# Optimization experiments

Hardware: AMD Instinct MI355X
Metric: run time of the kernel (lower is better)

## Reference

```python
import jax, jax.numpy as jnp
import numpy as np

N, E, F_IN, H, C = 169343, 1166243, 128, 128, 40
BN_EPS = 1e-5


def setup_inputs() -> dict:
    key = jax.random.key(0)
    ks = jax.random.split(key, 16)
    inp = {
        "x": jax.random.normal(ks[0], (N, F_IN), jnp.float32),
        "edge_index": jax.random.randint(ks[1], (2, E), 0, N, dtype=jnp.int64),
        "W1": jax.random.normal(ks[2], (F_IN, H), jnp.float32) * (1.0 / np.sqrt(F_IN)),
        "b1": jnp.zeros((H,), jnp.float32),
        "g1": jnp.ones((H,), jnp.float32),
        "be1": jnp.zeros((H,), jnp.float32),
        "m1": jax.random.normal(ks[3], (H,), jnp.float32) * 0.1,
        "v1": jax.random.uniform(ks[4], (H,), jnp.float32, 0.5, 1.5),
        "W2": jax.random.normal(ks[5], (H, H), jnp.float32) * (1.0 / np.sqrt(H)),
        "b2": jnp.zeros((H,), jnp.float32),
        "g2": jnp.ones((H,), jnp.float32),
        "be2": jnp.zeros((H,), jnp.float32),
        "m2": jax.random.normal(ks[6], (H,), jnp.float32) * 0.1,
        "v2": jax.random.uniform(ks[7], (H,), jnp.float32, 0.5, 1.5),
        "W3": jax.random.normal(ks[8], (H, C), jnp.float32) * (1.0 / np.sqrt(H)),
        "b3": jnp.zeros((C,), jnp.float32),
    }
    return inp


def _gcn_conv(h, W, b, src, dst, norm, n_nodes):
    # GCNConv: out = D^-1/2 (A+I) D^-1/2 (h W) + b
    hw = h @ W                                   # [N, H] dense GEMM
    msgs = hw[src] * norm[:, None]               # [E', H] gather (irregular)
    agg = jax.ops.segment_sum(msgs, dst, num_segments=n_nodes)  # scatter-add
    return agg + b


def _bn_eval(h, gamma, beta, mean, var):
    return (h - mean) * jax.lax.rsqrt(var + BN_EPS) * gamma + beta


def reference(x, edge_index, W1, b1, g1, be1, m1, v1,
              W2, b2, g2, be2, m2, v2, W3, b3):
    n = x.shape[0]
    loops = jnp.arange(n, dtype=edge_index.dtype)
    src = jnp.concatenate([edge_index[0], loops])  # add self-loops
    dst = jnp.concatenate([edge_index[1], loops])
    deg = jax.ops.segment_sum(jnp.ones_like(dst, dtype=x.dtype), dst, num_segments=n)
    dinv = jax.lax.rsqrt(jnp.maximum(deg, 1.0))
    norm = dinv[src] * dinv[dst]                  # [E+N]

    # layer stack (eval mode: dropout is identity, repeated ReLU idempotent)
    h = jax.nn.relu(_gcn_conv(x, W1, b1, src, dst, norm, n))
    h = jax.nn.relu(_bn_eval(h, g1, be1, m1, v1))
    h = jax.nn.relu(_gcn_conv(h, W2, b2, src, dst, norm, n))
    h = jax.nn.relu(_bn_eval(h, g2, be2, m2, v2))
    out = h @ W3 + b3                              # final Linear [N, C]
    return jax.nn.log_softmax(out, axis=-1), jnp.var(out, ddof=1)
```

## Files before the change

kernel.cpp:

```cpp
#include <hip/hip_runtime.h>
#include <math.h>

#define BN_EPS 1e-5f

typedef _Float16 f16;
typedef __attribute__((ext_vector_type(4))) _Float16 f16x4;
typedef __attribute__((ext_vector_type(8))) _Float16 f16x8;
typedef __attribute__((ext_vector_type(4))) float f32x4;

__device__ __forceinline__ int edge_at(const void* ei, long long idx, int is64) {
    if (is64) return (int)((const long long*)ei)[idx];
    return ((const int*)ei)[idx];
}

__global__ void init_kernel(const void* ei, int* flag, int* deg_i,
                            double* scal, int* done, int n) {
    int i = blockIdx.x * 256 + threadIdx.x;
    if (i < n) deg_i[i] = 0;
    if (blockIdx.x == 0 && threadIdx.x == 0) {
        scal[0] = 0.0; scal[1] = 0.0;
        *done = 0;
        const int* p = (const int*)ei;
        int f = 1;
        for (int k = 0; k < 64; k++)
            if (p[2 * k + 1] != 0) { f = 0; break; }
        *flag = f;
    }
}

__global__ void degi_kernel(const void* ei, const int* flag, int* deg_i,
                            int* __restrict__ rank, int E) {
    const int base = blockIdx.x * 1024 + threadIdx.x;
    const int is64 = *flag;
    #pragma unroll
    for (int k = 0; k < 4; k++) {
        int e = base + k * 256;
        if (e < E) {
            int d = edge_at(ei, (long long)E + e, is64);
            rank[e] = atomicAdd(&deg_i[d], 1);
        }
    }
}

__global__ __launch_bounds__(256) void scan1_kernel(
    const int* __restrict__ in, int* __restrict__ excl, int* bsum, int n) {
    __shared__ int sh[256];
    const int tid = threadIdx.x;
    const int base = blockIdx.x * 2048 + tid * 8;
    int v[8];
    #pragma unroll
    for (int i = 0; i < 8; i++) v[i] = (base + i < n) ? in[base + i] : 0;
    int tsum = 0;
    #pragma unroll
    for (int i = 0; i < 8; i++) { int t = v[i]; v[i] = tsum; tsum += t; }
    sh[tid] = tsum;
    __syncthreads();
    for (int off = 1; off < 256; off <<= 1) {
        int t = 0;
        if (tid >= off) t = sh[tid - off];
        __syncthreads();
        if (tid >= off) sh[tid] += t;
        __syncthreads();
    }
    int texcl = sh[tid] - tsum;
    #pragma unroll
    for (int i = 0; i < 8; i++)
        if (base + i < n) excl[base + i] = texcl + v[i];
    if (tid == 255 && bsum) bsum[blockIdx.x] = sh[255];
}

__global__ void scan3_kernel(int* rowptr, const int* __restrict__ boff,
                             const int* __restrict__ deg_i,
                             float* __restrict__ dinv, int n, int E) {
    int i = blockIdx.x * 256 + threadIdx.x;
    if (i < n) {
        rowptr[i] = rowptr[i] + boff[i >> 11];
        dinv[i] = rsqrtf((float)(deg_i[i] + 1));
    }
    if (i == 0) rowptr[n] = E;
}

__global__ void fill_kernel(const void* ei, const int* flag,
                            const int* __restrict__ rowptr,
                            const int* __restrict__ rank,
                            int* __restrict__ col, int E) {
    const int base = blockIdx.x * 1024 + threadIdx.x;
    const int is64 = *flag;
    #pragma unroll
    for (int k = 0; k < 4; k++) {
        int e = base + k * 256;
        if (e < E) {
            int s = edge_at(ei, e, is64);
            int d = edge_at(ei, (long long)E + e, is64);
            __builtin_nontemporal_store(s, &col[rowptr[d] + rank[e]]);
        }
    }
}

__global__ __launch_bounds__(256) void prep_w_kernel(
    const float* __restrict__ W1, f16* __restrict__ Wt1h, f16* __restrict__ Wt1l,
    const float* __restrict__ W2, f16* __restrict__ Wt2h, f16* __restrict__ Wt2l) {
    for (int f = blockIdx.x * 256 + threadIdx.x; f < 2 * 128 * 128;
         f += gridDim.x * 256) {
        int which = f >> 14, g = f & 16383;
        int k = g >> 7, nn = g & 127;
        const float* W = which ? W2 : W1;
        f16* Wh = which ? Wt2h : Wt1h;
        f16* Wl = which ? Wt2l : Wt1l;
        float wv = W[g];
        f16 h = (f16)wv;
        Wh[nn * 128 + k] = h;
        Wl[nn * 128 + k] = (f16)(wv - (float)h);
    }
}

#define APAD 40
__global__ __launch_bounds__(256) void gemm_l1_kernel(
    const float* __restrict__ X, const f16* __restrict__ Wth,
    const f16* __restrict__ Wtl, const float* __restrict__ dinv,
    f16* __restrict__ out, int M) {
    __shared__ f16 Ah[128 * APAD];
    __shared__ f16 Bh[128 * APAD];
    __shared__ f16 Bl[128 * APAD];
    const int t = threadIdx.x;
    const int r0 = blockIdx.x * 128;
    const int w = t >> 6, lane = t & 63;
    const int m0 = (w >> 1) * 64, n0 = (w & 1) * 64;
    const int fr = lane & 15;
    const int kb = (lane >> 4) * 8;

    f32x4 acc[4][4];
    #pragma unroll
    for (int i = 0; i < 4; i++)
        #pragma unroll
        for (int j = 0; j < 4; j++) acc[i][j] = (f32x4)0.f;

    for (int k0 = 0; k0 < 128; k0 += 32) {
        #pragma unroll
        for (int i = 0; i < 4; i++) {
            int f = t + i * 256;
            int row = f >> 3, kq = (f & 7) * 4;
            float4 v = make_float4(0.f, 0.f, 0.f, 0.f);
            if (r0 + row < M)
                v = *(const float4*)&X[(size_t)(r0 + row) * 128 + k0 + kq];
            *(f16x4*)&Ah[row * APAD + kq] =
                (f16x4){(f16)v.x, (f16)v.y, (f16)v.z, (f16)v.w};
        }
        #pragma unroll
        for (int i = 0; i < 2; i++) {
            int f = t + i * 256;
            int nrow = f >> 2, kq = (f & 3) * 8;
            int gb = nrow * 128 + k0 + kq;
            int lb = nrow * APAD + kq;
            *(uint4*)&Bh[lb] = *(const uint4*)&Wth[gb];
            *(uint4*)&Bl[lb] = *(const uint4*)&Wtl[gb];
        }
        __syncthreads();

        f16x8 a0[4], b0[4], xx[4];
        #pragma unroll
        for (int i = 0; i < 4; i++) {
            a0[i] = *(const f16x8*)&Ah[(m0 + i * 16 + fr) * APAD + kb];
            b0[i] = *(const f16x8*)&Bh[(n0 + i * 16 + fr) * APAD + kb];
        }
        #pragma unroll
        for (int i = 0; i < 4; i++)
            #pragma unroll
            for (int j = 0; j < 4; j++)
                acc[i][j] = __builtin_amdgcn_mfma_f32_16x16x32_f16(
                    a0[i], b0[j], acc[i][j], 0, 0, 0);
        #pragma unroll
        for (int i = 0; i < 4; i++)
            xx[i] = *(const f16x8*)&Bl[(n0 + i * 16 + fr) * APAD + kb];
        #pragma unroll
        for (int i = 0; i < 4; i++)
            #pragma unroll
            for (int j = 0; j < 4; j++)
                acc[i][j] = __builtin_amdgcn_mfma_f32_16x16x32_f16(
                    a0[i], xx[j], acc[i][j], 0, 0, 0);
        __syncthreads();
    }

    #pragma unroll
    for (int i = 0; i < 4; i++) {
        #pragma unroll
        for (int r = 0; r < 4; r++) {
            int row = r0 + m0 + i * 16 + (lane >> 4) * 4 + r;
            if (row < M) {
                float di = dinv[row];
                #pragma unroll
                for (int j = 0; j < 4; j++)
                    out[(size_t)row * 128 + n0 + j * 16 + fr] =
                        (f16)(acc[i][j][r] * di);
            }
        }
    }
}

__global__ __launch_bounds__(256) void gemm_l2_kernel(
    const f16* __restrict__ X, const f16* __restrict__ Wth,
    const f16* __restrict__ Wtl, const float* __restrict__ dinv,
    f16* __restrict__ out, int M) {
    __shared__ f16 Ax[128 * APAD];
    __shared__ f16 Bh[128 * APAD];
    __shared__ f16 Bl[128 * APAD];
    const int t = threadIdx.x;
    const int r0 = blockIdx.x * 128;
    const int w = t >> 6, lane = t & 63;
    const int m0 = (w >> 1) * 64, n0 = (w & 1) * 64;
    const int fr = lane & 15;
    const int kb = (lane >> 4) * 8;

    f32x4 acc[4][4];
    #pragma unroll
    for (int i = 0; i < 4; i++)
        #pragma unroll
        for (int j = 0; j < 4; j++) acc[i][j] = (f32x4)0.f;

    for (int k0 = 0; k0 < 128; k0 += 32) {
        #pragma unroll
        for (int i = 0; i < 2; i++) {
            int f = t + i * 256;
            int row = f >> 2, kq = (f & 3) * 8;
            uint4 v = make_uint4(0u, 0u, 0u, 0u);
            if (r0 + row < M)
                v = *(const uint4*)&X[(size_t)(r0 + row) * 128 + k0 + kq];
            *(uint4*)&Ax[row * APAD + kq] = v;
        }
        #pragma unroll
        for (int i = 0; i < 2; i++) {
            int f = t + i * 256;
            int nrow = f >> 2, kq = (f & 3) * 8;
            int gb = nrow * 128 + k0 + kq;
            int lb = nrow * APAD + kq;
            *(uint4*)&Bh[lb] = *(const uint4*)&Wth[gb];
            *(uint4*)&Bl[lb] = *(const uint4*)&Wtl[gb];
        }
        __syncthreads();

        f16x8 a0[4], b0[4], xx[4];
        #pragma unroll
        for (int i = 0; i < 4; i++) {
            a0[i] = *(const f16x8*)&Ax[(m0 + i * 16 + fr) * APAD + kb];
            b0[i] = *(const f16x8*)&Bh[(n0 + i * 16 + fr) * APAD + kb];
        }
        #pragma unroll
        for (int i = 0; i < 4; i++)
            #pragma unroll
            for (int j = 0; j < 4; j++)
                acc[i][j] = __builtin_amdgcn_mfma_f32_16x16x32_f16(
                    a0[i], b0[j], acc[i][j], 0, 0, 0);
        #pragma unroll
        for (int i = 0; i < 4; i++)
            xx[i] = *(const f16x8*)&Bl[(n0 + i * 16 + fr) * APAD + kb];
        #pragma unroll
        for (int i = 0; i < 4; i++)
            #pragma unroll
            for (int j = 0; j < 4; j++)
                acc[i][j] = __builtin_amdgcn_mfma_f32_16x16x32_f16(
                    a0[i], xx[j], acc[i][j], 0, 0, 0);
        __syncthreads();
    }

    #pragma unroll
    for (int i = 0; i < 4; i++) {
        #pragma unroll
        for (int r = 0; r < 4; r++) {
            int row = r0 + m0 + i * 16 + (lane >> 4) * 4 + r;
            if (row < M) {
                float di = dinv[row];
                #pragma unroll
                for (int j = 0; j < 4; j++)
                    out[(size_t)row * 128 + n0 + j * 16 + fr] =
                        (f16)(acc[i][j][r] * di);
            }
        }
    }
}

__global__ __launch_bounds__(256) void agg_kernel(
    const f16* __restrict__ hs, const int* __restrict__ rowptr,
    const int* __restrict__ col, const float* __restrict__ dinv,
    const float* __restrict__ b, const float* __restrict__ g,
    const float* __restrict__ be, const float* __restrict__ m,
    const float* __restrict__ v, f16* __restrict__ h, int M) {
    const int node = blockIdx.x * 8 + (threadIdx.x >> 5);
    if (node >= M) return;
    const int lane = threadIdx.x & 31;
    const int c = lane * 4;
    const f16* __restrict__ base = hs + c;

    f16x4 sv = *(const f16x4*)&base[(size_t)node * 128];
    float a0[4] = {(float)sv[0], (float)sv[1], (float)sv[2], (float)sv[3]};
    float a1[4] = {0.f, 0.f, 0.f, 0.f};
    float a2[4] = {0.f, 0.f, 0.f, 0.f};
    float a3[4] = {0.f, 0.f, 0.f, 0.f};
    const int beg = rowptr[node], end = rowptr[node + 1];
    int j = beg;
    for (; j + 3 < end; j += 4) {
        int s0 = col[j], s1 = col[j + 1], s2 = col[j + 2], s3 = col[j + 3];
        f16x4 v0 = *(const f16x4*)&base[(size_t)s0 * 128];
        f16x4 v1 = *(const f16x4*)&base[(size_t)s1 * 128];
        f16x4 v2 = *(const f16x4*)&base[(size_t)s2 * 128];
        f16x4 v3 = *(const f16x4*)&base[(size_t)s3 * 128];
        #pragma unroll
        for (int q = 0; q < 4; q++) {
            a0[q] += (float)v0[q]; a1[q] += (float)v1[q];
            a2[q] += (float)v2[q]; a3[q] += (float)v3[q];
        }
    }
    if (j + 1 < end) {
        int s0 = col[j], s1 = col[j + 1];
        f16x4 v0 = *(const f16x4*)&base[(size_t)s0 * 128];
        f16x4 v1 = *(const f16x4*)&base[(size_t)s1 * 128];
        #pragma unroll
        for (int q = 0; q < 4; q++) { a0[q] += (float)v0[q]; a1[q] += (float)v1[q]; }
        j += 2;
    }
    if (j < end) {
        int s0 = col[j];
        f16x4 v0 = *(const f16x4*)&base[(size_t)s0 * 128];
        #pragma unroll
        for (int q = 0; q < 4; q++) a0[q] += (float)v0[q];
    }
    const float di = dinv[node];
    f16x4 r;
    #pragma unroll
    for (int q = 0; q < 4; q++) {
        int cc = c + q;
        float s = (a0[q] + a1[q]) + (a2[q] + a3[q]);
        float tt = fmaxf(di * s + b[cc], 0.f);
        tt = (tt - m[cc]) * (g[cc] * rsqrtf(v[cc] + BN_EPS)) + be[cc];
        r[q] = (f16)fmaxf(tt, 0.f);
    }
    *(f16x4*)&h[(size_t)node * 128 + c] = r;
}

__global__ __launch_bounds__(256) void gemm_out_kernel(
    const f16* __restrict__ H, const float* __restrict__ W3,
    const float* __restrict__ b3, float* __restrict__ out,
    double* __restrict__ scal, int* __restrict__ done, int M) {
    __shared__ float Hs[256][20];
    __shared__ float Ws[128][40];
    const int t  = threadIdx.x;
    const int r0 = blockIdx.x * 256;
    #pragma unroll
    for (int i = 0; i < 5; i++) {
        int f = t + i * 256;
        ((float4*)Ws)[f] = ((const float4*)W3)[f];
    }
    const int rg = t >> 2;
    const int cb = (t & 3) * 10;
    float acc[4][10];
    #pragma unroll
    for (int i = 0; i < 4; i++)
        #pragma unroll
        for (int j = 0; j < 10; j++) acc[i][j] = 0.f;

    for (int k0 = 0; k0 < 128; k0 += 16) {
        __syncthreads();
        #pragma unroll
        for (int i = 0; i < 4; i++) {
            int f = t + i * 256;
            int r = f >> 2, c4 = (f & 3) * 4;
            float4 hv = make_float4(0.f, 0.f, 0.f, 0.f);
            if (r0 + r < M) {
                f16x4 hx = *(const f16x4*)&H[(size_t)(r0 + r) * 128 + k0 + c4];
                hv = make_float4((float)hx[0], (float)hx[1],
                                 (float)hx[2], (float)hx[3]);
            }
            *(float4*)&Hs[r][c4] = hv;
        }
        __syncthreads();
        #pragma unroll
        for (int k4 = 0; k4 < 4; k4++) {
            float hv[4][4];
            #pragma unroll
            for (int i = 0; i < 4; i++) {
                float4 h4 = *(const float4*)&Hs[rg + 64 * i][k4 * 4];
                hv[i][0] = h4.x; hv[i][1] = h4.y; hv[i][2] = h4.z; hv[i][3] = h4.w;
            }
            #pragma unroll
            for (int q = 0; q < 4; q++) {
                int k = k0 + k4 * 4 + q;
                float wv[10];
                #pragma unroll
                for (int j = 0; j < 5; j++) {
                    float2 w2 = *(const float2*)&Ws[k][cb + 2 * j];
                    wv[2 * j] = w2.x; wv[2 * j + 1] = w2.y;
                }
                #pragma unroll
                for (int i = 0; i < 4; i++)
                    #pragma unroll
                    for (int j = 0; j < 10; j++)
                        acc[i][j] = fmaf(hv[i][q], wv[j], acc[i][j]);
            }
        }
    }

    float s1 = 0.f, s2 = 0.f;
    #pragma unroll
    for (int i = 0; i < 4; i++) {
        int row = r0 + rg + 64 * i;
        float vb[10];
        #pragma unroll
        for (int j = 0; j < 10; j++) vb[j] = acc[i][j] + b3[cb + j];
        float mx = vb[0];
        #pragma unroll
        for (int j = 1; j < 10; j++) mx = fmaxf(mx, vb[j]);
        mx = fmaxf(mx, __shfl_xor(mx, 1));
        mx = fmaxf(mx, __shfl_xor(mx, 2));
        float se = 0.f;
        #pragma unroll
        for (int j = 0; j < 10; j++) se += expf(vb[j] - mx);
        se += __shfl_xor(se, 1);
        se += __shfl_xor(se, 2);
        float ls = mx + logf(se);
        if (row < M) {
            #pragma unroll
            for (int j = 0; j < 10; j++) {
                out[(size_t)row * 40 + cb + j] = vb[j] - ls;
                s1 += vb[j];
                s2 += vb[j] * vb[j];
            }
        }
    }
    #pragma unroll
    for (int o = 32; o; o >>= 1) { s1 += __shfl_xor(s1, o); s2 += __shfl_xor(s2, o); }
    __shared__ double sh1[4], sh2[4];
    if ((t & 63) == 0) { sh1[t >> 6] = (double)s1; sh2[t >> 6] = (double)s2; }
    __syncthreads();
    if (t == 0) {
        atomicAdd(&scal[0], sh1[0] + sh1[1] + sh1[2] + sh1[3]);
        atomicAdd(&scal[1], sh2[0] + sh2[1] + sh2[2] + sh2[3]);
        __threadfence();
        int prev = atomicAdd(done, 1);
        if (prev == (int)gridDim.x - 1) {
            __threadfence();
            double t1 = atomicAdd(&scal[0], 0.0);
            double t2 = atomicAdd(&scal[1], 0.0);
            long long nn = (long long)M * 40;
            out[nn] = (float)((t2 - t1 * t1 / (double)nn) / (double)(nn - 1));
        }
    }
}

extern "C" void kernel_launch(void* const* d_in, const int* in_sizes, int n_in,
                              void* d_out, int out_size, void* d_ws, size_t ws_size,
                              hipStream_t stream) {
    const float* x   = (const float*)d_in[0];
    const void*  ei  = d_in[1];
    const float* W1  = (const float*)d_in[2];
    const float* b1  = (const float*)d_in[3];
    const float* g1  = (const float*)d_in[4];
    const float* be1 = (const float*)d_in[5];
    const float* m1  = (const float*)d_in[6];
    const float* v1  = (const float*)d_in[7];
    const float* W2  = (const float*)d_in[8];
    const float* b2  = (const float*)d_in[9];
    const float* g2  = (const float*)d_in[10];
    const float* be2 = (const float*)d_in[11];
    const float* m2  = (const float*)d_in[12];
    const float* v2  = (const float*)d_in[13];
    const float* W3  = (const float*)d_in[14];
    const float* b3  = (const float*)d_in[15];

    const int n = in_sizes[0] / 128;
    const int E = in_sizes[1] / 2;
    float* out = (float*)d_out;

    size_t nh   = (size_t)n * 128;
    size_t npad = ((size_t)n + 3) & ~(size_t)3;
    size_t Epad = ((size_t)E + 3) & ~(size_t)3;
    double* scal   = (double*)d_ws;
    f16*    A      = (f16*)(scal + 2);
    f16*    B      = A + nh;
    float*  dinv   = (float*)(B + nh);
    int*    deg_i  = (int*)(dinv + npad);
    int*    rowptr = deg_i + npad;
    int*    rank   = rowptr + npad + 4;
    int*    bsum   = rank + Epad;
    int*    boff   = bsum + 128;
    int*    flag   = boff + 128;
    int*    done   = flag + 4;
    int*    col    = done + 4;
    f16*    Wt1h   = (f16*)(col + Epad);
    f16*    Wt1l   = Wt1h + 128 * 128;
    f16*    Wt2h   = Wt1l + 128 * 128;
    f16*    Wt2l   = Wt2h + 128 * 128;

    const int nb_n   = (n + 255) / 256;
    const int nb_e4  = (E + 1023) / 1024;
    const int nb_gm  = (n + 127) / 128;
    const int nb_agg = (n + 7) / 8;
    const int nb_g3  = (n + 255) / 256;
    const int nb_sc  = (n + 2047) / 2048;

    init_kernel<<<nb_n, 256, 0, stream>>>(ei, flag, deg_i, scal, done, n);
    degi_kernel<<<nb_e4, 256, 0, stream>>>(ei, flag, deg_i, rank, E);
    prep_w_kernel<<<128, 256, 0, stream>>>(W1, Wt1h, Wt1l, W2, Wt2h, Wt2l);

    scan1_kernel<<<nb_sc, 256, 0, stream>>>(deg_i, rowptr, bsum, n);
    scan1_kernel<<<1, 256, 0, stream>>>(bsum, boff, nullptr, nb_sc);
    scan3_kernel<<<nb_n, 256, 0, stream>>>(rowptr, boff, deg_i, dinv, n, E);
    fill_kernel<<<nb_e4, 256, 0, stream>>>(ei, flag, rowptr, rank, col, E);

    gemm_l1_kernel<<<nb_gm, 256, 0, stream>>>(x, Wt1h, Wt1l, dinv, A, n);
    agg_kernel<<<nb_agg, 256, 0, stream>>>(A, rowptr, col, dinv,
                                           b1, g1, be1, m1, v1, B, n);
    gemm_l2_kernel<<<nb_gm, 256, 0, stream>>>(B, Wt2h, Wt2l, dinv, A, n);
    agg_kernel<<<nb_agg, 256, 0, stream>>>(A, rowptr, col, dinv,
                                           b2, g2, be2, m2, v2, B, n);
    gemm_out_kernel<<<nb_g3, 256, 0, stream>>>(B, W3, b3, out, scal, done, n);
}
```

Baseline: 557.5 us.

## Use split-fp16 MFMA for final linear layer with fused log-softmax

Replaces the scalar FP32 FMA output GEMM (H@W3) with MFMA 16x16x32 f16 instructions. W3 is pre-split into high and low fp16 halves, transposed, and padded to 48 columns in the prep kernel. Log-softmax and the variance reduction are reworked to fit the MFMA accumulator layout. This aims to cut the ALU cost of the final layer, at the price of doubled MFMAs for precision, padded columns, and B fragments read from global memory instead of LDS.

```diff
diff --git a/kernel.cpp b/kernel.cpp
--- a/kernel.cpp
+++ b/kernel.cpp
@@ -99,18 +99,29 @@
 
 __global__ __launch_bounds__(256) void prep_w_kernel(
     const float* __restrict__ W1, f16* __restrict__ Wt1h, f16* __restrict__ Wt1l,
-    const float* __restrict__ W2, f16* __restrict__ Wt2h, f16* __restrict__ Wt2l) {
-    for (int f = blockIdx.x * 256 + threadIdx.x; f < 2 * 128 * 128;
+    const float* __restrict__ W2, f16* __restrict__ Wt2h, f16* __restrict__ Wt2l,
+    const float* __restrict__ W3, f16* __restrict__ Wt3h, f16* __restrict__ Wt3l) {
+    const int total = 2 * 16384 + 48 * 128;
+    for (int f = blockIdx.x * 256 + threadIdx.x; f < total;
          f += gridDim.x * 256) {
-        int which = f >> 14, g = f & 16383;
-        int k = g >> 7, nn = g & 127;
-        const float* W = which ? W2 : W1;
-        f16* Wh = which ? Wt2h : Wt1h;
-        f16* Wl = which ? Wt2l : Wt1l;
-        float wv = W[g];
-        f16 h = (f16)wv;
-        Wh[nn * 128 + k] = h;
-        Wl[nn * 128 + k] = (f16)(wv - (float)h);
+        if (f < 2 * 16384) {
+            int which = f >> 14, g = f & 16383;
+            int k = g >> 7, nn = g & 127;
+            const float* W = which ? W2 : W1;
+            f16* Wh = which ? Wt2h : Wt1h;
+            f16* Wl = which ? Wt2l : Wt1l;
+            float wv = W[g];
+            f16 h = (f16)wv;
+            Wh[nn * 128 + k] = h;
+            Wl[nn * 128 + k] = (f16)(wv - (float)h);
+        } else {
+            int g = f - 2 * 16384;
+            int nn = g >> 7, k = g & 127;
+            float wv = (nn < 40) ? W3[k * 40 + nn] : 0.f;
+            f16 h = (f16)wv;
+            Wt3h[g] = h;
+            Wt3l[g] = (f16)(wv - (float)h);
+        }
     }
 }
 
@@ -337,98 +348,107 @@
 }
 
 __global__ __launch_bounds__(256) void gemm_out_kernel(
-    const f16* __restrict__ H, const float* __restrict__ W3,
-    const float* __restrict__ b3, float* __restrict__ out,
-    double* __restrict__ scal, int* __restrict__ done, int M) {
-    __shared__ float Hs[256][20];
-    __shared__ float Ws[128][40];
-    const int t  = threadIdx.x;
-    const int r0 = blockIdx.x * 256;
-    #pragma unroll
-    for (int i = 0; i < 5; i++) {
-        int f = t + i * 256;
-        ((float4*)Ws)[f] = ((const float4*)W3)[f];
-    }
-    const int rg = t >> 2;
-    const int cb = (t & 3) * 10;
-    float acc[4][10];
-    #pragma unroll
-    for (int i = 0; i < 4; i++)
-        #pragma unroll
-        for (int j = 0; j < 10; j++) acc[i][j] = 0.f;
-
-    for (int k0 = 0; k0 < 128; k0 += 16) {
-        __syncthreads();
-        #pragma unroll
-        for (int i = 0; i < 4; i++) {
+    const f16* __restrict__ H, const f16* __restrict__ Wt3h,
+    const f16* __restrict__ Wt3l, const float* __restrict__ b3,
+    float* __restrict__ out, double* __restrict__ scal,
+    int* __restrict__ done, int M) {
+    __shared__ f16 Ax[128 * APAD];
+    const int t = threadIdx.x;
+    const int r0 = blockIdx.x * 128;
+    const int w = t >> 6, lane = t & 63;
+    const int m0 = w * 32;
+    const int fr = lane & 15;
+    const int kb = (lane >> 4) * 8;
+
+    f32x4 acc[2][3];
+    #pragma unroll
+    for (int i = 0; i < 2; i++)
+        #pragma unroll
+        for (int j = 0; j < 3; j++) acc[i][j] = (f32x4)0.f;
+
+    for (int k0 = 0; k0 < 128; k0 += 32) {
+        #pragma unroll
+        for (int i = 0; i < 2; i++) {
             int f = t + i * 256;
-            int r = f >> 2, c4 = (f & 3) * 4;
-            float4 hv = make_float4(0.f, 0.f, 0.f, 0.f);
-            if (r0 + r < M) {
-                f16x4 hx = *(const f16x4*)&H[(size_t)(r0 + r) * 128 + k0 + c4];
-                hv = make_float4((float)hx[0], (float)hx[1],
-                                 (float)hx[2], (float)hx[3]);
+            int row = f >> 2, kq = (f & 3) * 8;
+            uint4 v = make_uint4(0u, 0u, 0u, 0u);
+            if (r0 + row < M)
+                v = *(const uint4*)&H[(size_t)(r0 + row) * 128 + k0 + kq];
+            *(uint4*)&Ax[row * APAD + kq] = v;
+        }
+        __syncthreads();
+
+        f16x8 a0[2], bh[3], bl[3];
+        #pragma unroll
+        for (int i = 0; i < 2; i++)
+            a0[i] = *(const f16x8*)&Ax[(m0 + i * 16 + fr) * APAD + kb];
+        #pragma unroll
+        for (int j = 0; j < 3; j++) {
+            int gb = (j * 16 + fr) * 128 + k0 + kb;
+            bh[j] = *(const f16x8*)&Wt3h[gb];
+            bl[j] = *(const f16x8*)&Wt3l[gb];
+        }
+        #pragma unroll
+        for (int i = 0; i < 2; i++)
+            #pragma unroll
+            for (int j = 0; j < 3; j++) {
+                acc[i][j] = __builtin_amdgcn_mfma_f32_16x16x32_f16(
+                    a0[i], bh[j], acc[i][j], 0, 0, 0);
+                acc[i][j] = __builtin_amdgcn_mfma_f32_16x16x32_f16(
+                    a0[i], bl[j], acc[i][j], 0, 0, 0);
             }
-            *(float4*)&Hs[r][c4] = hv;
-        }
-        __syncthreads();
-        #pragma unroll
-        for (int k4 = 0; k4 < 4; k4++) {
-            float hv[4][4];
-            #pragma unroll
-            for (int i = 0; i < 4; i++) {
-                float4 h4 = *(const float4*)&Hs[rg + 64 * i][k4 * 4];
-                hv[i][0] = h4.x; hv[i][1] = h4.y; hv[i][2] = h4.z; hv[i][3] = h4.w;
+        __syncthreads();
+    }
+
+    float bb[3];
+    int cg[3];
+    #pragma unroll
+    for (int j = 0; j < 3; j++) {
+        cg[j] = j * 16 + fr;
+        bb[j] = (cg[j] < 40) ? b3[cg[j]] : 0.f;
+    }
+    float s1 = 0.f, s2 = 0.f;
+    #pragma unroll
+    for (int i = 0; i < 2; i++) {
+        #pragma unroll
+        for (int r = 0; r < 4; r++) {
+            int row = r0 + m0 + i * 16 + (lane >> 4) * 4 + r;
+            float vv[3];
+            float mx = -INFINITY;
+            #pragma unroll
+            for (int j = 0; j < 3; j++) {
+                vv[j] = acc[i][j][r] + bb[j];
+                if (cg[j] < 40) mx = fmaxf(mx, vv[j]);
             }
-            #pragma unroll
-            for (int q = 0; q < 4; q++) {
-                int k = k0 + k4 * 4 + q;
-                float wv[10];
+            mx = fmaxf(mx, __shfl_xor(mx, 1));
+            mx = fmaxf(mx, __shfl_xor(mx, 2));
+            mx = fmaxf(mx, __shfl_xor(mx, 4));
+            mx = fmaxf(mx, __shfl_xor(mx, 8));
+            float se = 0.f;
+            #pragma unroll
+            for (int j = 0; j < 3; j++)
+                if (cg[j] < 40) se += expf(vv[j] - mx);
+            se += __shfl_xor(se, 1);
+            se += __shfl_xor(se, 2);
+            se += __shfl_xor(se, 4);
+            se += __shfl_xor(se, 8);
+            float ls = mx + logf(se);
+            if (row < M) {
                 #pragma unroll
-                for (int j = 0; j < 5; j++) {
-                    float2 w2 = *(const float2*)&Ws[k][cb + 2 * j];
-                    wv[2 * j] = w2.x; wv[2 * j + 1] = w2.y;
+                for (int j = 0; j < 3; j++) {
+                    if (cg[j] < 40) {
+                        out[(size_t)row * 40 + cg[j]] = vv[j] - ls;
+                        s1 += vv[j];
+                        s2 += vv[j] * vv[j];
+                    }
                 }
-                #pragma unroll
-                for (int i = 0; i < 4; i++)
-                    #pragma unroll
-                    for (int j = 0; j < 10; j++)
-                        acc[i][j] = fmaf(hv[i][q], wv[j], acc[i][j]);
-            }
-        }
-    }
-
-    float s1 = 0.f, s2 = 0.f;
-    #pragma unroll
-    for (int i = 0; i < 4; i++) {
-        int row = r0 + rg + 64 * i;
-        float vb[10];
-        #pragma unroll
-        for (int j = 0; j < 10; j++) vb[j] = acc[i][j] + b3[cb + j];
-        float mx = vb[0];
-        #pragma unroll
-        for (int j = 1; j < 10; j++) mx = fmaxf(mx, vb[j]);
-        mx = fmaxf(mx, __shfl_xor(mx, 1));
-        mx = fmaxf(mx, __shfl_xor(mx, 2));
-        float se = 0.f;
-        #pragma unroll
-        for (int j = 0; j < 10; j++) se += expf(vb[j] - mx);
-        se += __shfl_xor(se, 1);
-        se += __shfl_xor(se, 2);
-        float ls = mx + logf(se);
-        if (row < M) {
-            #pragma unroll
-            for (int j = 0; j < 10; j++) {
-                out[(size_t)row * 40 + cb + j] = vb[j] - ls;
-                s1 += vb[j];
-                s2 += vb[j] * vb[j];
             }
         }
     }
     #pragma unroll
     for (int o = 32; o; o >>= 1) { s1 += __shfl_xor(s1, o); s2 += __shfl_xor(s2, o); }
     __shared__ double sh1[4], sh2[4];
-    if ((t & 63) == 0) { sh1[t >> 6] = (double)s1; sh2[t >> 6] = (double)s2; }
+    if (lane == 0) { sh1[w] = (double)s1; sh2[w] = (double)s2; }
     __syncthreads();
     if (t == 0) {
         atomicAdd(&scal[0], sh1[0] + sh1[1] + sh1[2] + sh1[3]);
@@ -488,17 +508,19 @@
     f16*    Wt1l   = Wt1h + 128 * 128;
     f16*    Wt2h   = Wt1l + 128 * 128;
     f16*    Wt2l   = Wt2h + 128 * 128;
+    f16*    Wt3h   = Wt2l + 128 * 128;
+    f16*    Wt3l   = Wt3h + 48 * 128;
 
     const int nb_n   = (n + 255) / 256;
     const int nb_e4  = (E + 1023) / 1024;
     const int nb_gm  = (n + 127) / 128;
     const int nb_agg = (n + 7) / 8;
-    const int nb_g3  = (n + 255) / 256;
     const int nb_sc  = (n + 2047) / 2048;
 
     init_kernel<<<nb_n, 256, 0, stream>>>(ei, flag, deg_i, scal, done, n);
     degi_kernel<<<nb_e4, 256, 0, stream>>>(ei, flag, deg_i, rank, E);
-    prep_w_kernel<<<128, 256, 0, stream>>>(W1, Wt1h, Wt1l, W2, Wt2h, Wt2l);
+    prep_w_kernel<<<160, 256, 0, stream>>>(W1, Wt1h, Wt1l, W2, Wt2h, Wt2l,
+                                           W3, Wt3h, Wt3l);
 
     scan1_kernel<<<nb_sc, 256, 0, stream>>>(deg_i, rowptr, bsum, n);
     scan1_kernel<<<1, 256, 0, stream>>>(bsum, boff, nullptr, nb_sc);
@@ -511,5 +533,6 @@
     gemm_l2_kernel<<<nb_gm, 256, 0, stream>>>(B, Wt2h, Wt2l, dinv, A, n);
     agg_kernel<<<nb_agg, 256, 0, stream>>>(A, rowptr, col, dinv,
                                            b2, g2, be2, m2, v2, B, n);
-    gemm_out_kernel<<<nb_g3, 256, 0, stream>>>(B, W3, b3, out, scal, done, n);
-}
+    gemm_out_kernel<<<nb_gm, 256, 0, stream>>>(B, Wt3h, Wt3l, b3, out,
+                                               scal, done, n);
+}
```

New measurement: 566.5 us. No clear change (+1.6%).
